# Performance work log

Measured on AMD Instinct MI355X. Metric: run time of the kernel, lower is better.

The kernel has to match this reference:

```python
import jax, jax.numpy as jnp
import numpy as np

N = 100000
DIM = 128
N_EDGES = 3200000
EPS = 1e-5


def setup_inputs() -> dict:
    key = jax.random.key(0)
    k1, k2, k3, k4, k5, k6 = jax.random.split(key, 6)
    x = jax.random.normal(k1, (N, DIM), dtype=jnp.float32)
    edge_row = jnp.sort(jax.random.randint(k2, (N_EDGES,), 0, N, dtype=jnp.int64))
    edge_col = jax.random.randint(k3, (N_EDGES,), 0, N, dtype=jnp.int64)
    edge_val = jax.random.uniform(k4, (N_EDGES,), dtype=jnp.float32)
    gamma = jnp.ones((DIM,), dtype=jnp.float32)
    beta = jnp.zeros((DIM,), dtype=jnp.float32)
    return {"x": x, "edge_row": edge_row, "edge_col": edge_col,
            "edge_val": edge_val, "gamma": gamma, "beta": beta}


def _layernorm(h, gamma, beta):
    mu = jnp.mean(h, axis=-1, keepdims=True)
    var = jnp.mean(jnp.square(h - mu), axis=-1, keepdims=True)
    return (h - mu) * jax.lax.rsqrt(var + EPS) * gamma + beta


def reference(x, edge_row, edge_col, edge_val, gamma, beta):
    # sparse adj @ x  ==  segment-sum of val * x[src] into dst rows
    msgs = edge_val[:, None] * x[edge_col]            # [E, DIM]
    h = jax.ops.segment_sum(msgs, edge_row, num_segments=N)  # [N, DIM]
    return _layernorm(h + x, gamma, beta)
```

## Files before the change

kernel.cpp:

```cpp
#include <hip/hip_runtime.h>
#include <hip/hip_fp16.h>

#define DIM 128
#define EPS 1e-5f
#define WPB 4
#define UF  4

#define WBOUND 6.5f

typedef float vfloat2 __attribute__((ext_vector_type(2)));

#if __has_builtin(__builtin_amdgcn_sdot4)
#define SDOT4(a, b, c) __builtin_amdgcn_sdot4((a), (b), (c), false)
#else
static __device__ __forceinline__ int SDOT4(int a, int b, int c)
{
#pragma unroll
    for (int k = 0; k < 4; ++k)
        c += ((a << (24 - 8 * k)) >> 24) * ((b << (24 - 8 * k)) >> 24);
    return c;
}
#endif

__global__ void quant_kernel(const float4* __restrict__ x4,
                             unsigned int* __restrict__ x8,
                             float*        __restrict__ scales,
                             int n_nodes)
{
    const int t   = blockIdx.x * blockDim.x + threadIdx.x;
    const int row = t >> 5;
    if (row >= n_nodes) return;

    const float4 v = x4[t];
    float m = fmaxf(fmaxf(fabsf(v.x), fabsf(v.y)),
                    fmaxf(fabsf(v.z), fabsf(v.w)));
#pragma unroll
    for (int off = 1; off <= 16; off <<= 1)
        m = fmaxf(m, __shfl_xor(m, off, 64));

    const float inv = (m > 0.f) ? 127.f / m : 0.f;
    const int q0 = __float2int_rn(v.x * inv);
    const int q1 = __float2int_rn(v.y * inv);
    const int q2 = __float2int_rn(v.z * inv);
    const int q3 = __float2int_rn(v.w * inv);
    x8[t] = ((unsigned)(q0 & 0xFF))        | ((unsigned)(q1 & 0xFF) << 8) |
            ((unsigned)(q2 & 0xFF) << 16)  | ((unsigned)(q3 & 0xFF) << 24);

    if ((threadIdx.x & 31) == 0)
        scales[row] = m * (1.f / 127.f);
}

__global__ void csr_w8_kernel(const int*   __restrict__ edge_row,
                              const int*   __restrict__ edge_col,
                              const float* __restrict__ edge_val,
                              const float* __restrict__ scales,
                              int*          __restrict__ row_ptr,
                              unsigned char* __restrict__ w8,
                              int n_nodes, int n_edges)
{
    int i = blockIdx.x * blockDim.x + threadIdx.x;
    if (i >= n_edges) return;

    const float ws = edge_val[i] * scales[edge_col[i]];
    int wq = __float2int_rn(ws * (16129.f / WBOUND));
    wq = min(wq, 127);
    w8[i] = (unsigned char)wq;

    int cur  = edge_row[i];
    int prev = (i == 0) ? -1 : edge_row[i - 1];
    for (int r = prev + 1; r <= cur; ++r) row_ptr[r] = i;
    if (i == n_edges - 1) {
        for (int r = cur + 1; r <= n_nodes; ++r) row_ptr[r] = n_edges;
    }
}

template<bool MASKED>
__device__ __forceinline__
void edge_trip(int e0, int q, int sub, int start, unsigned len, int emax,
               const uint2* __restrict__ x8,
               const int*   __restrict__ edge_col,
               const unsigned char* __restrict__ w8,
               int acc[8])
{
    const int b  = e0 + 4 * q;
    const int bc = MASKED ? min(b, emax) : b;
    int4     c4 = *(const int4*)(edge_col + bc);
    unsigned wd = *(const unsigned*)(w8 + bc);

    int c[UF] = {c4.x, c4.y, c4.z, c4.w};

    if (MASKED) {
        const int off = b - start;
        const int p = min(max(0, -off), 3);
        const int v = min(max((int)len - off, 0), 4);
        const unsigned pmask = 0xFFFFFFFFu << (8 * p);
        const unsigned smask = (v >= 4) ? 0xFFFFFFFFu
                                        : ((1u << (8 * v)) - 1u);
        wd &= pmask & smask;
#pragma unroll
        for (int u = 0; u < UF; ++u) {
            bool in = (unsigned)(off + u) < len;
            c[u] = in ? c[u] : 0;
        }
    }

    const uint2 v0 = x8[c[0] * (DIM / 8) + sub];
    const uint2 v1 = x8[c[1] * (DIM / 8) + sub];
    const uint2 v2 = x8[c[2] * (DIM / 8) + sub];
    const uint2 v3 = x8[c[3] * (DIM / 8) + sub];

    unsigned ab01 = __builtin_amdgcn_perm(v1.x, v0.x, 0x05010400u);
    unsigned ab23 = __builtin_amdgcn_perm(v1.x, v0.x, 0x07030602u);
    unsigned cd01 = __builtin_amdgcn_perm(v3.x, v2.x, 0x05010400u);
    unsigned cd23 = __builtin_amdgcn_perm(v3.x, v2.x, 0x07030602u);
    unsigned t0 = __builtin_amdgcn_perm(cd01, ab01, 0x05040100u);
    unsigned t1 = __builtin_amdgcn_perm(cd01, ab01, 0x07060302u);
    unsigned t2 = __builtin_amdgcn_perm(cd23, ab23, 0x05040100u);
    unsigned t3 = __builtin_amdgcn_perm(cd23, ab23, 0x07060302u);
    unsigned ab45 = __builtin_amdgcn_perm(v1.y, v0.y, 0x05010400u);
    unsigned ab67 = __builtin_amdgcn_perm(v1.y, v0.y, 0x07030602u);
    unsigned cd45 = __builtin_amdgcn_perm(v3.y, v2.y, 0x05010400u);
    unsigned cd67 = __builtin_amdgcn_perm(v3.y, v2.y, 0x07030602u);
    unsigned t4 = __builtin_amdgcn_perm(cd45, ab45, 0x05040100u);
    unsigned t5 = __builtin_amdgcn_perm(cd45, ab45, 0x07060302u);
    unsigned t6 = __builtin_amdgcn_perm(cd67, ab67, 0x05040100u);
    unsigned t7 = __builtin_amdgcn_perm(cd67, ab67, 0x07060302u);

    acc[0] = SDOT4((int)wd, (int)t0, acc[0]);
    acc[1] = SDOT4((int)wd, (int)t1, acc[1]);
    acc[2] = SDOT4((int)wd, (int)t2, acc[2]);
    acc[3] = SDOT4((int)wd, (int)t3, acc[3]);
    acc[4] = SDOT4((int)wd, (int)t4, acc[4]);
    acc[5] = SDOT4((int)wd, (int)t5, acc[5]);
    acc[6] = SDOT4((int)wd, (int)t6, acc[6]);
    acc[7] = SDOT4((int)wd, (int)t7, acc[7]);
}

__global__ __launch_bounds__(WPB * 64)
void gnn_fused_kernel(const uint2* __restrict__ x8,
                      const float* __restrict__ scales,
                      const int*   __restrict__ row_ptr,
                      const int*   __restrict__ edge_col,
                      const unsigned char* __restrict__ w8,
                      const float* __restrict__ gamma,
                      const float* __restrict__ beta,
                      float*       __restrict__ out,
                      int n_nodes, int n_edges)
{
    const int wave = threadIdx.x >> 6;
    const int lane = threadIdx.x & 63;
    const int q    = lane >> 4;
    const int sub  = lane & 15;
    const int node = blockIdx.x * WPB + wave;
    if (node >= n_nodes) return;

    const int start = row_ptr[node];
    const int end   = row_ptr[node + 1];
    const unsigned len = (unsigned)(end - start);

    const uint2 xr = x8[node * (DIM / 8) + sub];
    const float sn = scales[node];

    int acc[8];
#pragma unroll
    for (int k = 0; k < 8; ++k) acc[k] = 0;

    const int ebase = start & ~3;
    const int emax  = n_edges - 4;

    if (ebase < end) {
        edge_trip<true>(ebase, q, sub, start, len, emax,
                        x8, edge_col, w8, acc);
        int e0 = ebase + 4 * UF;
        for (; e0 + 4 * UF <= end; e0 += 4 * UF)
            edge_trip<false>(e0, q, sub, start, len, emax,
                             x8, edge_col, w8, acc);
        if (e0 < end)
            edge_trip<true>(e0, q, sub, start, len, emax,
                            x8, edge_col, w8, acc);
    }

#pragma unroll
    for (int k = 0; k < 8; ++k) {
        acc[k] += __shfl_xor(acc[k], 16, 64);
        acc[k] += __shfl_xor(acc[k], 32, 64);
    }

    const float s_w = WBOUND / 16129.f;
    const int rlo = (int)xr.x, rhi = (int)xr.y;
    float h[8];
    h[0] = fmaf(sn, (float)((rlo << 24) >> 24), s_w * (float)acc[0]);
    h[1] = fmaf(sn, (float)((rlo << 16) >> 24), s_w * (float)acc[1]);
    h[2] = fmaf(sn, (float)((rlo <<  8) >> 24), s_w * (float)acc[2]);
    h[3] = fmaf(sn, (float)( rlo        >> 24), s_w * (float)acc[3]);
    h[4] = fmaf(sn, (float)((rhi << 24) >> 24), s_w * (float)acc[4]);
    h[5] = fmaf(sn, (float)((rhi << 16) >> 24), s_w * (float)acc[5]);
    h[6] = fmaf(sn, (float)((rhi <<  8) >> 24), s_w * (float)acc[6]);
    h[7] = fmaf(sn, (float)( rhi        >> 24), s_w * (float)acc[7]);

    float s = 0.f, sq = 0.f;
#pragma unroll
    for (int k = 0; k < 8; ++k) { s += h[k]; sq += h[k] * h[k]; }
#pragma unroll
    for (int off = 1; off <= 8; off <<= 1) {
        s  += __shfl_xor(s,  off, 64);
        sq += __shfl_xor(sq, off, 64);
    }
    const float mean = s * (1.0f / (float)DIM);
    const float var  = sq * (1.0f / (float)DIM) - mean * mean;
    const float rs   = rsqrtf(var + EPS);

    float hx = (q < 2) ? ((q == 0) ? h[0] : h[2]) : ((q == 2) ? h[4] : h[6]);
    float hy = (q < 2) ? ((q == 0) ? h[1] : h[3]) : ((q == 2) ? h[5] : h[7]);
    const int didx = sub * 4 + q;
    const float2 g = ((const float2*)gamma)[didx];
    const float2 b = ((const float2*)beta)[didx];
    vfloat2 o;
    o.x = (hx - mean) * rs * g.x + b.x;
    o.y = (hy - mean) * rs * g.y + b.y;
    __builtin_nontemporal_store(o, (vfloat2*)out + node * (DIM / 2) + didx);
}

extern "C" void kernel_launch(void* const* d_in, const int* in_sizes, int n_in,
                              void* d_out, int out_size, void* d_ws, size_t ws_size,
                              hipStream_t stream)
{
    const float* x        = (const float*)d_in[0];
    const int*   edge_row = (const int*)  d_in[1];
    const int*   edge_col = (const int*)  d_in[2];
    const float* edge_val = (const float*)d_in[3];
    const float* gamma    = (const float*)d_in[4];
    const float* beta     = (const float*)d_in[5];
    float*       out      = (float*)d_out;

    const int n_nodes = in_sizes[0] / DIM;
    const int n_edges = in_sizes[1];
    const int n_elem  = in_sizes[0];

    unsigned char* wsb = (unsigned char*)d_ws;
    unsigned int*  x8      = (unsigned int*)wsb;
    int*           row_ptr = (int*)  (wsb + (size_t)n_elem);
    float*         scales  = (float*)(wsb + (size_t)n_elem
                                      + (size_t)(n_nodes + 1) * sizeof(int));
    unsigned char* w8      = wsb + (size_t)n_elem
                             + (size_t)(n_nodes + 1) * sizeof(int)
                             + (size_t)n_nodes * sizeof(float);

    const int qthreads = n_nodes * (DIM / 4);
    quant_kernel<<<(qthreads + 255) / 256, 256, 0, stream>>>(
        (const float4*)x, x8, scales, n_nodes);
    csr_w8_kernel<<<(n_edges + 255) / 256, 256, 0, stream>>>(
        edge_row, edge_col, edge_val, scales, row_ptr, w8, n_nodes, n_edges);

    const int blocks = (n_nodes + WPB - 1) / WPB;
    gnn_fused_kernel<<<blocks, WPB * 64, 0, stream>>>(
        (const uint2*)x8, scales, row_ptr, edge_col, w8,
        gamma, beta, out, n_nodes, n_edges);
}
```

Baseline: 212.5 us.

## Software-pipeline edge gathers with inline-asm loads and explicit vmcnt waits

```diff
diff --git a/kernel.cpp b/kernel.cpp
--- a/kernel.cpp
+++ b/kernel.cpp
@@ -4,11 +4,11 @@
 #define DIM 128
 #define EPS 1e-5f
 #define WPB 4
-#define UF  4
-
 #define WBOUND 6.5f
 
-typedef float vfloat2 __attribute__((ext_vector_type(2)));
+typedef float    vfloat2 __attribute__((ext_vector_type(2)));
+typedef int      int4v   __attribute__((ext_vector_type(4)));
+typedef unsigned uint2v  __attribute__((ext_vector_type(2)));
 
 #if __has_builtin(__builtin_amdgcn_sdot4)
 #define SDOT4(a, b, c) __builtin_amdgcn_sdot4((a), (b), (c), false)
@@ -21,6 +21,9 @@
     return c;
 }
 #endif
+
+#define WAITV(n) do { asm volatile("s_waitcnt vmcnt(" #n ")"); \
+                      __builtin_amdgcn_sched_barrier(0); } while (0)
 
 __global__ void quant_kernel(const float4* __restrict__ x4,
                              unsigned int* __restrict__ x8,
@@ -74,41 +77,50 @@
     }
 }
 
-template<bool MASKED>
 __device__ __forceinline__
-void edge_trip(int e0, int q, int sub, int start, unsigned len, int emax,
-               const uint2* __restrict__ x8,
-               const int*   __restrict__ edge_col,
-               const unsigned char* __restrict__ w8,
-               int acc[8])
-{
-    const int b  = e0 + 4 * q;
-    const int bc = MASKED ? min(b, emax) : b;
-    int4     c4 = *(const int4*)(edge_col + bc);
-    unsigned wd = *(const unsigned*)(w8 + bc);
-
-    int c[UF] = {c4.x, c4.y, c4.z, c4.w};
-
-    if (MASKED) {
-        const int off = b - start;
+void load_edges_asm(const int* __restrict__ ec,
+                    const unsigned char* __restrict__ w8,
+                    int bc, int4v& c4, unsigned& wd)
+{
+    unsigned long ca = (unsigned long)(const void*)(ec + bc);
+    unsigned long wa = (unsigned long)(const void*)(w8 + bc);
+    asm volatile("global_load_dwordx4 %0, %1, off" : "=&v"(c4) : "v"(ca));
+    asm volatile("global_load_dword %0, %1, off"   : "=&v"(wd) : "v"(wa));
+}
+
+__device__ __forceinline__
+void issue_gathers_asm(unsigned long xbase, const int c[4], uint2v v[4])
+{
+#pragma unroll
+    for (int u = 0; u < 4; ++u) {
+        unsigned long a = xbase + ((unsigned long)(unsigned)c[u] << 7);
+        asm volatile("global_load_dwordx2 %0, %1, off" : "=&v"(v[u]) : "v"(a));
+    }
+}
+
+__device__ __forceinline__
+void mask_edges(const int4v rc, unsigned rw, int off, unsigned len,
+                bool edge_mask, int c[4], unsigned& wd)
+{
+    c[0] = rc.x; c[1] = rc.y; c[2] = rc.z; c[3] = rc.w; wd = rw;
+    if (edge_mask) {
         const int p = min(max(0, -off), 3);
         const int v = min(max((int)len - off, 0), 4);
         const unsigned pmask = 0xFFFFFFFFu << (8 * p);
-        const unsigned smask = (v >= 4) ? 0xFFFFFFFFu
-                                        : ((1u << (8 * v)) - 1u);
+        const unsigned smask = (v >= 4) ? 0xFFFFFFFFu : ((1u << (8 * v)) - 1u);
         wd &= pmask & smask;
 #pragma unroll
-        for (int u = 0; u < UF; ++u) {
+        for (int u = 0; u < 4; ++u) {
             bool in = (unsigned)(off + u) < len;
             c[u] = in ? c[u] : 0;
         }
     }
-
-    const uint2 v0 = x8[c[0] * (DIM / 8) + sub];
-    const uint2 v1 = x8[c[1] * (DIM / 8) + sub];
-    const uint2 v2 = x8[c[2] * (DIM / 8) + sub];
-    const uint2 v3 = x8[c[3] * (DIM / 8) + sub];
-
+}
+
+__device__ __forceinline__
+void dot_trip(const uint2v v0, const uint2v v1, const uint2v v2,
+              const uint2v v3, unsigned wd, int acc[8])
+{
     unsigned ab01 = __builtin_amdgcn_perm(v1.x, v0.x, 0x05010400u);
     unsigned ab23 = __builtin_amdgcn_perm(v1.x, v0.x, 0x07030602u);
     unsigned cd01 = __builtin_amdgcn_perm(v3.x, v2.x, 0x05010400u);
@@ -136,7 +148,7 @@
     acc[7] = SDOT4((int)wd, (int)t7, acc[7]);
 }
 
-__global__ __launch_bounds__(WPB * 64)
+__global__ __launch_bounds__(WPB * 64, 8)
 void gnn_fused_kernel(const uint2* __restrict__ x8,
                       const float* __restrict__ scales,
                       const int*   __restrict__ row_ptr,
@@ -160,6 +172,7 @@
 
     const uint2 xr = x8[node * (DIM / 8) + sub];
     const float sn = scales[node];
+    asm volatile("" :: "v"(xr.x), "v"(xr.y), "v"(sn));
 
     int acc[8];
 #pragma unroll
@@ -168,16 +181,67 @@
     const int ebase = start & ~3;
     const int emax  = n_edges - 4;
 
-    if (ebase < end) {
-        edge_trip<true>(ebase, q, sub, start, len, emax,
-                        x8, edge_col, w8, acc);
-        int e0 = ebase + 4 * UF;
-        for (; e0 + 4 * UF <= end; e0 += 4 * UF)
-            edge_trip<false>(e0, q, sub, start, len, emax,
-                             x8, edge_col, w8, acc);
-        if (e0 < end)
-            edge_trip<true>(e0, q, sub, start, len, emax,
-                            x8, edge_col, w8, acc);
+    if (len > 0) {
+        const int T = (end - ebase + 15) >> 4;
+        const unsigned long xbase =
+            (unsigned long)(const void*)x8 + ((unsigned)sub << 3);
+        const int bq = 4 * q;
+
+        int4v rcA, rcB; unsigned rwA, rwB;
+        int cA[4], cB[4]; unsigned wdA, wdB;
+        uint2v vA[4], vB[4];
+
+        const int b0 = ebase + bq;
+        load_edges_asm(edge_col, w8, min(b0, emax), rcA, rwA);
+        WAITV(0);
+        mask_edges(rcA, rwA, b0 - start, len, true, cA, wdA);
+        if (T > 1)
+            load_edges_asm(edge_col, w8, min(b0 + 16, emax), rcB, rwB);
+        issue_gathers_asm(xbase, cA, vA);
+
+        int t = 0;
+        for (;;) {
+            if (t + 1 < T) {
+                WAITV(4);
+                const int bn = ebase + 16 * (t + 1) + bq;
+                mask_edges(rcB, rwB, bn - start, len, (t + 1 == T - 1),
+                           cB, wdB);
+                if (t + 2 < T) {
+                    load_edges_asm(edge_col, w8, min(bn + 16, emax), rcA, rwA);
+                    issue_gathers_asm(xbase, cB, vB);
+                    WAITV(6);
+                } else {
+                    issue_gathers_asm(xbase, cB, vB);
+                    WAITV(4);
+                }
+                dot_trip(vA[0], vA[1], vA[2], vA[3], wdA, acc);
+                ++t;
+            } else {
+                WAITV(0);
+                dot_trip(vA[0], vA[1], vA[2], vA[3], wdA, acc);
+                break;
+            }
+            if (t + 1 < T) {
+                WAITV(4);
+                const int bn = ebase + 16 * (t + 1) + bq;
+                mask_edges(rcA, rwA, bn - start, len, (t + 1 == T - 1),
+                           cA, wdA);
+                if (t + 2 < T) {
+                    load_edges_asm(edge_col, w8, min(bn + 16, emax), rcB, rwB);
+                    issue_gathers_asm(xbase, cA, vA);
+                    WAITV(6);
+                } else {
+                    issue_gathers_asm(xbase, cA, vA);
+                    WAITV(4);
+                }
+                dot_trip(vB[0], vB[1], vB[2], vB[3], wdB, acc);
+                ++t;
+            } else {
+                WAITV(0);
+                dot_trip(vB[0], vB[1], vB[2], vB[3], wdB, acc);
+                break;
+            }
+        }
     }
 
 #pragma unroll
```

After: 231.5 us. 8.9% more time.
